# Optimization experiments

Hardware: AMD Instinct MI355X
Metric: run time of the kernel (lower is better)

Reference implementation:

```python
import jax, jax.numpy as jnp
import numpy as np

B, CIN, COUT, DK, DV, NH, H, W = 8, 256, 512, 256, 256, 8, 32, 32
DKH = DK // NH  # 32
DVH = DV // NH  # 32


def _conv(x, w, b, pad):
    y = jax.lax.conv_general_dilated(
        x, w, window_strides=(1, 1), padding=[(pad, pad), (pad, pad)],
        dimension_numbers=('NCHW', 'OIHW', 'NCHW'))
    return y + b[None, :, None, None]


def setup_inputs() -> dict:
    key = jax.random.key(0)
    ks = jax.random.split(key, 6)
    s = jnp.float32(0.05)
    return {
        'x': jax.random.normal(ks[0], (B, CIN, H, W), jnp.float32),
        'w_conv': jax.random.normal(ks[1], (COUT - DV, CIN, 3, 3), jnp.float32) * s,
        'b_conv': jnp.zeros((COUT - DV,), jnp.float32),
        'w_qkv': jax.random.normal(ks[2], (2 * DK + DV, CIN, 3, 3), jnp.float32) * s,
        'b_qkv': jnp.zeros((2 * DK + DV,), jnp.float32),
        'w_att': jax.random.normal(ks[3], (DV, DV, 1, 1), jnp.float32) * s,
        'b_att': jnp.zeros((DV,), jnp.float32),
        'key_rel_w': jax.random.normal(ks[4], (2 * W - 1, DKH), jnp.float32),
        'key_rel_h': jax.random.normal(ks[5], (2 * H - 1, DKH), jnp.float32),
    }


def reference(x, w_conv, b_conv, w_qkv, b_qkv, w_att, b_att, key_rel_w, key_rel_h):
    qkv = _conv(x, w_qkv, b_qkv, 1)                 # (B, 2*DK+DV, H, W)
    b = x.shape[0]
    q, k, v = qkv[:, :DK], qkv[:, DK:2 * DK], qkv[:, 2 * DK:]
    q = q.reshape(b, NH, DKH, H, W) * (DKH ** -0.5)
    kf = k.reshape(b, NH, DKH, H * W)
    vf = v.reshape(b, NH, DVH, H * W)
    qf = q.reshape(b, NH, DKH, H * W)
    # content logits: (B, NH, HW, HW)
    logits = jnp.einsum('bhdm,bhdn->bhmn', qf, kf)
    # relative position logits (equivalent to the pad/reshape/slice skew trick)
    q5 = jnp.transpose(q, (0, 1, 3, 4, 2))          # (B, NH, H, W, DKH)
    rel_w = jnp.einsum('bhxyd,md->bhxym', q5, key_rel_w)   # (B,NH,H,W,2W-1)
    idx_w = (jnp.arange(W)[None, :] - jnp.arange(W)[:, None]) + (W - 1)  # idx[y,y']
    rel_w = jnp.take_along_axis(rel_w, idx_w[None, None, None], axis=-1)  # (B,NH,H,W,W) [x,y,y']
    rel_h = jnp.einsum('bhxyd,md->bhxym', q5, key_rel_h)   # (B,NH,H,W,2H-1)
    idx_h = (jnp.arange(H)[None, :] - jnp.arange(H)[:, None]) + (H - 1)  # idx[x,x']
    rel_h = jnp.take_along_axis(rel_h, idx_h[None, None, :, None, :], axis=-1)  # (B,NH,H,W,H) [x,y,x']
    # logits6 axes: [x, y, x', y']
    logits6 = (logits.reshape(b, NH, H, W, H, W)
               + rel_w[:, :, :, :, None, :]
               + rel_h[:, :, :, :, :, None])
    weights = jax.nn.softmax(logits6.reshape(b, NH, H * W, H * W), axis=-1)
    att = jnp.einsum('bhmn,bhdn->bhmd', weights, vf)  # (B, NH, HW, DVH)
    # faithful to torch's contiguous .view(batch, dim_v, H, W)
    att = att.reshape(b, DV, H, W)
    att = _conv(att, w_att, b_att, 0)
    xo = _conv(x, w_conv, b_conv, 1)
    return jnp.concatenate([xo, att], axis=1)
```

## Files before the change

### kernel.cpp

```cpp
#include <hip/hip_runtime.h>


typedef __attribute__((ext_vector_type(8))) short short8;
typedef __attribute__((ext_vector_type(4))) float floatx4;

__device__ __forceinline__ unsigned short f2bf(float f) {
    unsigned int u = __float_as_uint(f);
    u += 0x7FFFu + ((u >> 16) & 1u);
    return (unsigned short)(u >> 16);
}
__device__ __forceinline__ float bf2f(unsigned short s) {
    return __uint_as_float(((unsigned int)s) << 16);
}
__device__ __forceinline__ unsigned int pk2bf_trunc(float lo, float hi) {
    return (__float_as_uint(lo) >> 16) | (__float_as_uint(hi) & 0xFFFF0000u);
}
__device__ __forceinline__ unsigned int pk2bf_rne(float lo, float hi) {
    return (unsigned int)f2bf(lo) | ((unsigned int)f2bf(hi) << 16);
}
__device__ __forceinline__ void gload_lds16(const unsigned short* g, unsigned short* s) {
    __builtin_amdgcn_global_load_lds(
        (const __attribute__((address_space(1))) unsigned int*)g,
        (__attribute__((address_space(3))) unsigned int*)s, 16, 0, 0);
}

__global__ __launch_bounds__(256) void k_xt(const float* __restrict__ x,
                                            unsigned short* __restrict__ Xt) {
    __shared__ unsigned short lds[256 * 33];
    const int tid = threadIdx.x;
    const int yy = blockIdx.x % 34;
    const int b  = blockIdx.x / 34;
    unsigned int* outp = (unsigned int*)(Xt + (((size_t)b * 34 + yy) * 34) * 256);
    if (yy == 0 || yy == 33) {
        for (int i = tid; i < 4352; i += 256) outp[i] = 0;
        return;
    }
    const int y = yy - 1;
    const float* xb = x + (size_t)b * 262144 + y * 32;
#pragma unroll
    for (int it = 0; it < 32; ++it) {
        const int e = it * 256 + tid;
        const int ci = e >> 5, xx = e & 31;
        lds[ci * 33 + xx] = f2bf(xb[ci * 1024 + xx]);
    }
    __syncthreads();
    const int ci2 = (tid & 127) * 2;
    const int xh = tid >> 7;
#pragma unroll
    for (int it = 0; it < 17; ++it) {
        const int xx = xh * 17 + it;
        unsigned int v = 0;
        if (xx >= 1 && xx <= 32)
            v = (unsigned int)lds[ci2 * 33 + xx - 1] |
                ((unsigned int)lds[(ci2 + 1) * 33 + xx - 1] << 16);
        outp[xx * 128 + (tid & 127)] = v;
    }
}

__global__ __launch_bounds__(256) void k_wconv(const float* __restrict__ wc,
                                               const float* __restrict__ wq,
                                               const float* __restrict__ wa,
                                               const float* __restrict__ krw,
                                               const float* __restrict__ krh,
                                               unsigned short* __restrict__ wt,
                                               unsigned short* __restrict__ wt2,
                                               unsigned short* __restrict__ krwb,
                                               unsigned short* __restrict__ krhb) {
    const int tid = threadIdx.x;
    const int blk = blockIdx.x;
    if (blk < 1024) {
        __shared__ float lw[2304];
        const int n = blk;
        const float* src = (n < 256) ? (wc + (size_t)n * 2304)
                                     : (wq + (size_t)(n - 256) * 2304);
#pragma unroll
        for (int it = 0; it < 9; ++it)
            lw[it * 256 + tid] = src[it * 256 + tid];
        __syncthreads();
#pragma unroll
        for (int it = 0; it < 9; ++it) {
            const int kp = it * 256 + tid;
            const int g = kp >> 8, ci = kp & 255;
            wt[(size_t)n * 2304 + kp] = f2bf(lw[ci * 9 + g]);
        }
    } else {
        const int i = (blk - 1024) * 256 + tid;
        if (i < 65536)        wt2[i] = f2bf(wa[i]);
        else if (i < 67584) { const int j = i - 65536;
                              krwb[j] = (j < 2016) ? f2bf(krw[j]) : (unsigned short)0; }
        else if (i < 69632) { const int j = i - 67584;
                              krhb[j] = (j < 2016) ? f2bf(krh[j]) : (unsigned short)0; }
    }
}

__global__ __launch_bounds__(256, 4) void k_gemm0(const unsigned short* __restrict__ Wr,
                                                  const unsigned short* __restrict__ Xt,
                                                  float* __restrict__ out,
                                                  unsigned short* __restrict__ qT,
                                                  unsigned short* __restrict__ kT,
                                                  unsigned short* __restrict__ vT,
                                                  const float* __restrict__ bias_a,
                                                  const float* __restrict__ bias_b) {
    __shared__ unsigned short As[64 * 64];
    __shared__ unsigned short Bs[128 * 64];
    const int tid = threadIdx.x;
    const int lane = tid & 63, wv = tid >> 6;
    const int l15 = lane & 15, quad = lane >> 4;
    const int m0 = blockIdx.x * 128, n0 = blockIdx.y * 64;
    const int wave_m = (wv & 1) * 64, wave_n = (wv >> 1) * 32;
    floatx4 acc[2][4] = {};
    const int lr = lane >> 3;
    const int swz8 = ((lane & 7) ^ lr) * 8;
    const unsigned short* gA = Wr + (size_t)(n0 + wv * 16 + lr) * 2304 + swz8;
    int bb0[4];
#pragma unroll
    for (int r = 0; r < 4; ++r) {
        const int m = m0 + wv * 32 + r * 8 + lr;
        const int b = m >> 10, p = m & 1023, y = p >> 5, x = p & 31;
        bb0[r] = ((b * 34 + y) * 34 + x) * 256;
    }
    unsigned short* sA0 = As + wv * 1024;
    unsigned short* sB0 = Bs + wv * 2048;
    const int sw0 = ((quad)     ^ (l15 & 7)) * 8;
    const int sw1 = ((4 + quad) ^ (l15 & 7)) * 8;
    for (int k0 = 0; k0 < 2304; k0 += 64) {
        const int g = k0 >> 8;
        const int ci0 = k0 & 255;
        const int ky = g / 3, kx = g - ky * 3;
        const int offu = (ky * 34 + kx) * 256 + ci0 + swz8;
        __syncthreads();
        gload_lds16(gA + k0, sA0);
        gload_lds16(gA + (size_t)8 * 2304 + k0, sA0 + 512);
#pragma unroll
        for (int r = 0; r < 4; ++r)
            gload_lds16(Xt + bb0[r] + offu, sB0 + r * 512);
        __syncthreads();
#pragma unroll
        for (int h = 0; h < 2; ++h) {
            const int sw = h ? sw1 : sw0;
            short8 a[2], b[4];
#pragma unroll
            for (int i = 0; i < 2; ++i)
                a[i] = *reinterpret_cast<const short8*>(As + (wave_n + i * 16 + l15) * 64 + sw);
#pragma unroll
            for (int j = 0; j < 4; ++j)
                b[j] = *reinterpret_cast<const short8*>(Bs + (wave_m + j * 16 + l15) * 64 + sw);
#pragma unroll
            for (int i = 0; i < 2; ++i)
#pragma unroll
                for (int j = 0; j < 4; ++j)
                    acc[i][j] = __builtin_amdgcn_mfma_f32_16x16x32_bf16(a[i], b[j], acc[i][j], 0, 0, 0);
        }
    }
#pragma unroll
    for (int i = 0; i < 2; ++i)
#pragma unroll
        for (int jj = 0; jj < 4; ++jj)
#pragma unroll
            for (int rg = 0; rg < 4; ++rg) {
                const int n = n0 + wave_n + i * 16 + quad * 4 + rg;
                const int m = m0 + wave_m + jj * 16 + l15;
                const float v = acc[i][jj][rg];
                const int bb = m >> 10, p = m & 1023;
                if (n < 256) {
                    out[(size_t)bb * 524288 + (size_t)n * 1024 + p] = v + bias_a[n];
                } else {
                    const int c = n - 256;
                    const float vq = v + bias_b[c];
                    if (c < 256) {
                        const int h = c >> 5, d = c & 31;
                        qT[(((size_t)(bb * 8 + h)) * 1024 + p) * 32 + d] =
                            f2bf(vq * 0.17677669529663687f);
                    } else if (c < 512) {
                        const int c2 = c - 256;
                        const int h = c2 >> 5, d = c2 & 31;
                        kT[(((size_t)(bb * 8 + h)) * 1024 + p) * 32 + d] = f2bf(vq);
                    } else {
                        const int c2 = c - 512;
                        const int h = c2 >> 5, d = c2 & 31;
                        vT[(((size_t)(bb * 8 + h)) * 32 + d) * 1024 + p] = f2bf(vq);
                    }
                }
            }
}

__global__ __launch_bounds__(256, 4) void k_attn(const unsigned short* __restrict__ qT,
                                                 const unsigned short* __restrict__ kT,
                                                 const unsigned short* __restrict__ vT,
                                                 const unsigned short* __restrict__ krwb,
                                                 const unsigned short* __restrict__ krhb,
                                                 unsigned short* __restrict__ attT) {
    __shared__ float rh_s[64 * 68];
    __shared__ unsigned short Pw[4 * 1152];
    const int tid = threadIdx.x;
    const int lane = tid & 63, wv = tid >> 6;
    const int l15 = lane & 15, quad = lane >> 4;
    const int bid = blockIdx.x;
    const int bh = bid & 63;
    const int qt = bid >> 6;
    const int h = bh & 7;
    const int b = bh >> 3;
    const unsigned short* qbase = qT + (size_t)bh * 32768;
    const unsigned short* kbase = kT + (size_t)bh * 32768;
    const unsigned short* vbase = vT + (size_t)bh * 32768;
    const int qloc = wv * 16 + l15;
    const int pq = qt * 64 + qloc;
    const int yq = pq >> 5, xq = pq & 31;

    const short8 qfrag = *reinterpret_cast<const short8*>(
        qbase + (size_t)pq * 32 + quad * 8);
    const floatx4 zero = {0.f, 0.f, 0.f, 0.f};
    unsigned short* pw = Pw + wv * 1152;

#pragma unroll
    for (int sub = 0; sub < 4; ++sub) {
        const short8 aw = *reinterpret_cast<const short8*>(krwb + (sub * 16 + l15) * 32 + quad * 8);
        const short8 ah = *reinterpret_cast<const short8*>(krhb + (sub * 16 + l15) * 32 + quad * 8);
        const floatx4 dw = __builtin_amdgcn_mfma_f32_16x16x32_bf16(aw, qfrag, zero, 0, 0, 0);
        const floatx4 dh = __builtin_amdgcn_mfma_f32_16x16x32_bf16(ah, qfrag, zero, 0, 0, 0);
        *reinterpret_cast<floatx4*>(rh_s + qloc * 68 + sub * 16 + quad * 4) = dh;
        uint2 uu;
        uu.x = pk2bf_rne(dw[0], dw[1]);
        uu.y = pk2bf_rne(dw[2], dw[3]);
        *reinterpret_cast<uint2*>(pw + l15 * 64 + sub * 16 + quad * 4) = uu;
    }
    float rwreg[8];
#pragma unroll
    for (int j = 0; j < 8; ++j) {
        const int xn = (j >> 2) * 16 + quad * 4 + (j & 3);
        rwreg[j] = bf2f(pw[l15 * 64 + xn - xq + 31]);
    }
    asm volatile("s_waitcnt lgkmcnt(0)" ::: "memory");

    const float* rhq = rh_s + qloc * 68 + 31 - yq;
    float lsum = 0.f;
    floatx4 O0 = zero, O1 = zero;

    short8 kf[4], vf[4];
#pragma unroll
    for (int sub = 0; sub < 4; ++sub)
        kf[sub] = *reinterpret_cast<const short8*>(
            kbase + (size_t)(sub * 16 + l15) * 32 + quad * 8);
#pragma unroll
    for (int n2 = 0; n2 < 2; ++n2) {
        vf[n2 * 2 + 0] = *reinterpret_cast<const short8*>(
            vbase + (size_t)l15 * 1024 + n2 * 32 + quad * 8);
        vf[n2 * 2 + 1] = *reinterpret_cast<const short8*>(
            vbase + (size_t)(16 + l15) * 1024 + n2 * 32 + quad * 8);
    }

#pragma unroll
    for (int nt = 0; nt < 16; ++nt) {
        const int n0 = nt * 64;
        const int n0n = (nt < 15) ? n0 + 64 : n0;
        floatx4 d[4];
#pragma unroll
        for (int sub = 0; sub < 4; ++sub)
            d[sub] = __builtin_amdgcn_mfma_f32_16x16x32_bf16(kf[sub], qfrag, zero, 0, 0, 0);
        short8 kfn[4], vfn[4];
#pragma unroll
        for (int sub = 0; sub < 4; ++sub)
            kfn[sub] = *reinterpret_cast<const short8*>(
                kbase + (size_t)(n0n + sub * 16 + l15) * 32 + quad * 8);
        const float rh0 = rhq[nt * 2];
        const float rh1 = rhq[nt * 2 + 1];
        float p[16];
#pragma unroll
        for (int sub = 0; sub < 4; ++sub) {
            const float rhv = (sub >> 1) ? rh1 : rh0;
#pragma unroll
            for (int r = 0; r < 4; ++r) {
                const float e = __expf(d[sub][r] + rwreg[(sub & 1) * 4 + r] + rhv);
                p[sub * 4 + r] = e;
                lsum += e;
            }
        }
#pragma unroll
        for (int sub = 0; sub < 4; ++sub) {
            uint2 uu;
            uu.x = pk2bf_trunc(p[sub * 4 + 0], p[sub * 4 + 1]);
            uu.y = pk2bf_trunc(p[sub * 4 + 2], p[sub * 4 + 3]);
            *reinterpret_cast<uint2*>(pw + l15 * 72 + sub * 16 + quad * 4) = uu;
        }
        asm volatile("s_waitcnt lgkmcnt(0)" ::: "memory");
#pragma unroll
        for (int n2 = 0; n2 < 2; ++n2) {
            const short8 pfrag = *reinterpret_cast<const short8*>(
                pw + l15 * 72 + n2 * 32 + quad * 8);
            O0 = __builtin_amdgcn_mfma_f32_16x16x32_bf16(vf[n2 * 2 + 0], pfrag, O0, 0, 0, 0);
            O1 = __builtin_amdgcn_mfma_f32_16x16x32_bf16(vf[n2 * 2 + 1], pfrag, O1, 0, 0, 0);
        }
#pragma unroll
        for (int n2 = 0; n2 < 2; ++n2) {
            vfn[n2 * 2 + 0] = *reinterpret_cast<const short8*>(
                vbase + (size_t)l15 * 1024 + n0n + n2 * 32 + quad * 8);
            vfn[n2 * 2 + 1] = *reinterpret_cast<const short8*>(
                vbase + (size_t)(16 + l15) * 1024 + n0n + n2 * 32 + quad * 8);
        }
#pragma unroll
        for (int i = 0; i < 4; ++i) { kf[i] = kfn[i]; vf[i] = vfn[i]; }
    }
    lsum += __shfl_xor(lsum, 16);
    lsum += __shfl_xor(lsum, 32);
    const float inv = 1.0f / lsum;
    unsigned short* ob = attT + ((size_t)(h * 32 + yq)) * 8192 + b * 1024 + xq * 32;
    uint2 o0, o1;
    o0.x = pk2bf_rne(O0[0] * inv, O0[1] * inv);
    o0.y = pk2bf_rne(O0[2] * inv, O0[3] * inv);
    o1.x = pk2bf_rne(O1[0] * inv, O1[1] * inv);
    o1.y = pk2bf_rne(O1[2] * inv, O1[3] * inv);
    *reinterpret_cast<uint2*>(ob + quad * 4) = o0;
    *reinterpret_cast<uint2*>(ob + 16 + quad * 4) = o1;
}

__global__ __launch_bounds__(256) void k_tr(const unsigned short* __restrict__ src,
                                            unsigned short* __restrict__ dst) {
    __shared__ unsigned short t[64 * 72];
    const int tid = threadIdx.x;
    const int m0 = (blockIdx.x & 127) * 64;
    const int k0 = (blockIdx.x >> 7) * 64;
#pragma unroll
    for (int i = 0; i < 2; ++i) {
        const int idx = i * 256 + tid;
        const int k = idx >> 3, c8 = (idx & 7) * 8;
        *reinterpret_cast<uint4*>(t + k * 72 + c8) =
            *reinterpret_cast<const uint4*>(src + (size_t)(k0 + k) * 8192 + m0 + c8);
    }
    __syncthreads();
#pragma unroll
    for (int i = 0; i < 2; ++i) {
        const int idx = i * 256 + tid;
        const int m = idx >> 3, c8 = (idx & 7) * 8;
        unsigned short v[8];
#pragma unroll
        for (int j = 0; j < 8; ++j) v[j] = t[(c8 + j) * 72 + m];
        *reinterpret_cast<uint4*>(dst + (size_t)(m0 + m) * 256 + k0 + c8) =
            *reinterpret_cast<uint4*>(v);
    }
}

__global__ __launch_bounds__(256) void k_gemm_s(const unsigned short* __restrict__ Wm,
                                                const unsigned short* __restrict__ Dm,
                                                float* __restrict__ out,
                                                const float* __restrict__ bias) {
    __shared__ unsigned short As[64 * 40];
    __shared__ unsigned short Bs[64 * 40];
    const int tid = threadIdx.x;
    const int m0 = blockIdx.x * 64, n0 = blockIdx.y * 64;
    const int lane = tid & 63;
    const int wv = tid >> 6;
    const int l15 = lane & 15, quad = lane >> 4;
    const int n_off = (wv & 1) * 32, m_off = (wv >> 1) * 32;
    floatx4 acc[2][2] = {};
    const int r = tid >> 2, c8 = (tid & 3) * 8;
    const unsigned short* gA = Wm + (size_t)(n0 + r) * 256 + c8;
    const unsigned short* gB = Dm + (size_t)(m0 + r) * 256 + c8;
    unsigned short* sA = As + r * 40 + c8;
    unsigned short* sB = Bs + r * 40 + c8;
    for (int k0 = 0; k0 < 256; k0 += 32) {
        __syncthreads();
        *reinterpret_cast<uint4*>(sA) = *reinterpret_cast<const uint4*>(gA + k0);
        *reinterpret_cast<uint4*>(sB) = *reinterpret_cast<const uint4*>(gB + k0);
        __syncthreads();
        const short8 a0 = *reinterpret_cast<const short8*>(As + (n_off +      l15) * 40 + quad * 8);
        const short8 a1 = *reinterpret_cast<const short8*>(As + (n_off + 16 + l15) * 40 + quad * 8);
        const short8 b0 = *reinterpret_cast<const short8*>(Bs + (m_off +      l15) * 40 + quad * 8);
        const short8 b1 = *reinterpret_cast<const short8*>(Bs + (m_off + 16 + l15) * 40 + quad * 8);
        acc[0][0] = __builtin_amdgcn_mfma_f32_16x16x32_bf16(a0, b0, acc[0][0], 0, 0, 0);
        acc[0][1] = __builtin_amdgcn_mfma_f32_16x16x32_bf16(a0, b1, acc[0][1], 0, 0, 0);
        acc[1][0] = __builtin_amdgcn_mfma_f32_16x16x32_bf16(a1, b0, acc[1][0], 0, 0, 0);
        acc[1][1] = __builtin_amdgcn_mfma_f32_16x16x32_bf16(a1, b1, acc[1][1], 0, 0, 0);
    }
#pragma unroll
    for (int i = 0; i < 2; ++i)
#pragma unroll
        for (int jj = 0; jj < 2; ++jj)
#pragma unroll
            for (int rg = 0; rg < 4; ++rg) {
                const int n = n0 + n_off + i * 16 + quad * 4 + rg;
                const int m = m0 + m_off + jj * 16 + l15;
                const int bb = m >> 10, p = m & 1023;
                out[(size_t)bb * 524288 + (size_t)(n + 256) * 1024 + p] =
                    acc[i][jj][rg] + bias[n];
            }
}

extern "C" void kernel_launch(void* const* d_in, const int* in_sizes, int n_in,
                              void* d_out, int out_size, void* d_ws, size_t ws_size,
                              hipStream_t stream) {
    const float* x      = (const float*)d_in[0];
    const float* w_conv = (const float*)d_in[1];
    const float* b_conv = (const float*)d_in[2];
    const float* w_qkv  = (const float*)d_in[3];
    const float* b_qkv  = (const float*)d_in[4];
    const float* w_att  = (const float*)d_in[5];
    const float* b_att  = (const float*)d_in[6];
    const float* krw    = (const float*)d_in[7];
    const float* krh    = (const float*)d_in[8];
    float* out = (float*)d_out;

    char* ws = (char*)d_ws;
    unsigned short* Xt    = (unsigned short*)(ws);
    unsigned short* wt    = (unsigned short*)(ws + 9470464);
    unsigned short* wt2   = (unsigned short*)(ws + 14189056);
    unsigned short* qT    = (unsigned short*)(ws + 14320128);
    unsigned short* kT    = (unsigned short*)(ws + 18514432);
    unsigned short* vT    = (unsigned short*)(ws + 22708736);
    unsigned short* attt  = (unsigned short*)(ws + 26903040);
    unsigned short* krwb  = (unsigned short*)(ws + 31097344);
    unsigned short* krhb  = (unsigned short*)(ws + 31101440);
    unsigned short* attTT = (unsigned short*)(ws + 31105536);

    k_xt<<<dim3(272), dim3(256), 0, stream>>>(x, Xt);
    k_wconv<<<dim3(1296), dim3(256), 0, stream>>>(w_conv, w_qkv, w_att, krw, krh,
                                                  wt, wt2, krwb, krhb);
    k_gemm0<<<dim3(64, 16), dim3(256), 0, stream>>>(wt, Xt, out, qT, kT, vT,
                                                    b_conv, b_qkv);
    k_attn<<<dim3(1024), dim3(256), 0, stream>>>(qT, kT, vT, krwb, krhb, attTT);
    k_tr<<<dim3(512), dim3(256), 0, stream>>>(attTT, attt);
    k_gemm_s<<<dim3(128, 4), dim3(256), 0, stream>>>(wt2, attt, out, b_att);
}
```

Measured before the change: 196.5 us.

## Merge prep kernels and process two key tiles per attention iteration

```diff
diff --git a/kernel.cpp b/kernel.cpp
--- a/kernel.cpp
+++ b/kernel.cpp
@@ -24,53 +24,52 @@
         (__attribute__((address_space(3))) unsigned int*)s, 16, 0, 0);
 }
 
-__global__ __launch_bounds__(256) void k_xt(const float* __restrict__ x,
-                                            unsigned short* __restrict__ Xt) {
-    __shared__ unsigned short lds[256 * 33];
-    const int tid = threadIdx.x;
-    const int yy = blockIdx.x % 34;
-    const int b  = blockIdx.x / 34;
-    unsigned int* outp = (unsigned int*)(Xt + (((size_t)b * 34 + yy) * 34) * 256);
-    if (yy == 0 || yy == 33) {
-        for (int i = tid; i < 4352; i += 256) outp[i] = 0;
-        return;
-    }
-    const int y = yy - 1;
-    const float* xb = x + (size_t)b * 262144 + y * 32;
-#pragma unroll
-    for (int it = 0; it < 32; ++it) {
-        const int e = it * 256 + tid;
-        const int ci = e >> 5, xx = e & 31;
-        lds[ci * 33 + xx] = f2bf(xb[ci * 1024 + xx]);
-    }
-    __syncthreads();
-    const int ci2 = (tid & 127) * 2;
-    const int xh = tid >> 7;
-#pragma unroll
-    for (int it = 0; it < 17; ++it) {
-        const int xx = xh * 17 + it;
-        unsigned int v = 0;
-        if (xx >= 1 && xx <= 32)
-            v = (unsigned int)lds[ci2 * 33 + xx - 1] |
-                ((unsigned int)lds[(ci2 + 1) * 33 + xx - 1] << 16);
-        outp[xx * 128 + (tid & 127)] = v;
-    }
-}
-
-__global__ __launch_bounds__(256) void k_wconv(const float* __restrict__ wc,
-                                               const float* __restrict__ wq,
-                                               const float* __restrict__ wa,
-                                               const float* __restrict__ krw,
-                                               const float* __restrict__ krh,
-                                               unsigned short* __restrict__ wt,
-                                               unsigned short* __restrict__ wt2,
-                                               unsigned short* __restrict__ krwb,
-                                               unsigned short* __restrict__ krhb) {
+__global__ __launch_bounds__(256) void k_prep(const float* __restrict__ x,
+                                              const float* __restrict__ wc,
+                                              const float* __restrict__ wq,
+                                              const float* __restrict__ wa,
+                                              const float* __restrict__ krw,
+                                              const float* __restrict__ krh,
+                                              unsigned short* __restrict__ Xt,
+                                              unsigned short* __restrict__ wt,
+                                              unsigned short* __restrict__ wt2,
+                                              unsigned short* __restrict__ krwb,
+                                              unsigned short* __restrict__ krhb) {
+    __shared__ char smem[16896];
     const int tid = threadIdx.x;
     const int blk = blockIdx.x;
-    if (blk < 1024) {
-        __shared__ float lw[2304];
-        const int n = blk;
+    if (blk < 272) {
+        unsigned short* lds = (unsigned short*)smem;
+        const int yy = blk % 34;
+        const int b  = blk / 34;
+        unsigned int* outp = (unsigned int*)(Xt + (((size_t)b * 34 + yy) * 34) * 256);
+        if (yy == 0 || yy == 33) {
+            for (int i = tid; i < 4352; i += 256) outp[i] = 0;
+            return;
+        }
+        const int y = yy - 1;
+        const float* xb = x + (size_t)b * 262144 + y * 32;
+#pragma unroll
+        for (int it = 0; it < 32; ++it) {
+            const int e = it * 256 + tid;
+            const int ci = e >> 5, xx = e & 31;
+            lds[ci * 33 + xx] = f2bf(xb[ci * 1024 + xx]);
+        }
+        __syncthreads();
+        const int ci2 = (tid & 127) * 2;
+        const int xh = tid >> 7;
+#pragma unroll
+        for (int it = 0; it < 17; ++it) {
+            const int xx = xh * 17 + it;
+            unsigned int v = 0;
+            if (xx >= 1 && xx <= 32)
+                v = (unsigned int)lds[ci2 * 33 + xx - 1] |
+                    ((unsigned int)lds[(ci2 + 1) * 33 + xx - 1] << 16);
+            outp[xx * 128 + (tid & 127)] = v;
+        }
+    } else if (blk < 1296) {
+        float* lw = (float*)smem;
+        const int n = blk - 272;
         const float* src = (n < 256) ? (wc + (size_t)n * 2304)
                                      : (wq + (size_t)(n - 256) * 2304);
 #pragma unroll
@@ -84,7 +83,7 @@
             wt[(size_t)n * 2304 + kp] = f2bf(lw[ci * 9 + g]);
         }
     } else {
-        const int i = (blk - 1024) * 256 + tid;
+        const int i = (blk - 1296) * 256 + tid;
         if (i < 65536)        wt2[i] = f2bf(wa[i]);
         else if (i < 67584) { const int j = i - 65536;
                               krwb[j] = (j < 2016) ? f2bf(krw[j]) : (unsigned short)0; }
@@ -191,7 +190,7 @@
                                                  const unsigned short* __restrict__ krhb,
                                                  unsigned short* __restrict__ attT) {
     __shared__ float rh_s[64 * 68];
-    __shared__ unsigned short Pw[4 * 1152];
+    __shared__ unsigned short Pw[4 * 2304];
     const int tid = threadIdx.x;
     const int lane = tid & 63, wv = tid >> 6;
     const int l15 = lane & 15, quad = lane >> 4;
@@ -210,7 +209,8 @@
     const short8 qfrag = *reinterpret_cast<const short8*>(
         qbase + (size_t)pq * 32 + quad * 8);
     const floatx4 zero = {0.f, 0.f, 0.f, 0.f};
-    unsigned short* pw = Pw + wv * 1152;
+    unsigned short* pwA = Pw + wv * 2304;
+    unsigned short* pwB = pwA + 1152;
 
 #pragma unroll
     for (int sub = 0; sub < 4; ++sub) {
@@ -222,13 +222,13 @@
         uint2 uu;
         uu.x = pk2bf_rne(dw[0], dw[1]);
         uu.y = pk2bf_rne(dw[2], dw[3]);
-        *reinterpret_cast<uint2*>(pw + l15 * 64 + sub * 16 + quad * 4) = uu;
+        *reinterpret_cast<uint2*>(pwA + l15 * 64 + sub * 16 + quad * 4) = uu;
     }
     float rwreg[8];
 #pragma unroll
     for (int j = 0; j < 8; ++j) {
         const int xn = (j >> 2) * 16 + quad * 4 + (j & 3);
-        rwreg[j] = bf2f(pw[l15 * 64 + xn - xq + 31]);
+        rwreg[j] = bf2f(pwA[l15 * 64 + xn - xq + 31]);
     }
     asm volatile("s_waitcnt lgkmcnt(0)" ::: "memory");
 
@@ -236,69 +236,89 @@
     float lsum = 0.f;
     floatx4 O0 = zero, O1 = zero;
 
-    short8 kf[4], vf[4];
-#pragma unroll
-    for (int sub = 0; sub < 4; ++sub)
-        kf[sub] = *reinterpret_cast<const short8*>(
+    short8 kfa[4], kfb[4], vfa[4], vfb[4];
+#pragma unroll
+    for (int sub = 0; sub < 4; ++sub) {
+        kfa[sub] = *reinterpret_cast<const short8*>(
             kbase + (size_t)(sub * 16 + l15) * 32 + quad * 8);
-#pragma unroll
-    for (int n2 = 0; n2 < 2; ++n2) {
-        vf[n2 * 2 + 0] = *reinterpret_cast<const short8*>(
-            vbase + (size_t)l15 * 1024 + n2 * 32 + quad * 8);
-        vf[n2 * 2 + 1] = *reinterpret_cast<const short8*>(
-            vbase + (size_t)(16 + l15) * 1024 + n2 * 32 + quad * 8);
-    }
-
-#pragma unroll
-    for (int nt = 0; nt < 16; ++nt) {
-        const int n0 = nt * 64;
-        const int n0n = (nt < 15) ? n0 + 64 : n0;
-        floatx4 d[4];
+        kfb[sub] = *reinterpret_cast<const short8*>(
+            kbase + (size_t)(64 + sub * 16 + l15) * 32 + quad * 8);
+    }
+    vfa[0] = *reinterpret_cast<const short8*>(vbase + (size_t)l15 * 1024 + quad * 8);
+    vfa[1] = *reinterpret_cast<const short8*>(vbase + (size_t)(16 + l15) * 1024 + quad * 8);
+    vfa[2] = *reinterpret_cast<const short8*>(vbase + (size_t)l15 * 1024 + 32 + quad * 8);
+    vfa[3] = *reinterpret_cast<const short8*>(vbase + (size_t)(16 + l15) * 1024 + 32 + quad * 8);
+    vfb[0] = *reinterpret_cast<const short8*>(vbase + (size_t)l15 * 1024 + 64 + quad * 8);
+    vfb[1] = *reinterpret_cast<const short8*>(vbase + (size_t)(16 + l15) * 1024 + 64 + quad * 8);
+    vfb[2] = *reinterpret_cast<const short8*>(vbase + (size_t)l15 * 1024 + 96 + quad * 8);
+    vfb[3] = *reinterpret_cast<const short8*>(vbase + (size_t)(16 + l15) * 1024 + 96 + quad * 8);
+
+    for (int it = 0; it < 8; ++it) {
+        const int n0a = it * 128;
+        floatx4 da[4], db[4];
 #pragma unroll
         for (int sub = 0; sub < 4; ++sub)
-            d[sub] = __builtin_amdgcn_mfma_f32_16x16x32_bf16(kf[sub], qfrag, zero, 0, 0, 0);
-        short8 kfn[4], vfn[4];
+            da[sub] = __builtin_amdgcn_mfma_f32_16x16x32_bf16(kfa[sub], qfrag, zero, 0, 0, 0);
 #pragma unroll
         for (int sub = 0; sub < 4; ++sub)
-            kfn[sub] = *reinterpret_cast<const short8*>(
-                kbase + (size_t)(n0n + sub * 16 + l15) * 32 + quad * 8);
-        const float rh0 = rhq[nt * 2];
-        const float rh1 = rhq[nt * 2 + 1];
-        float p[16];
+            db[sub] = __builtin_amdgcn_mfma_f32_16x16x32_bf16(kfb[sub], qfrag, zero, 0, 0, 0);
+        const int nk = (it < 7) ? n0a + 128 : n0a;
 #pragma unroll
         for (int sub = 0; sub < 4; ++sub) {
-            const float rhv = (sub >> 1) ? rh1 : rh0;
-#pragma unroll
-            for (int r = 0; r < 4; ++r) {
-                const float e = __expf(d[sub][r] + rwreg[(sub & 1) * 4 + r] + rhv);
-                p[sub * 4 + r] = e;
-                lsum += e;
-            }
-        }
+            kfa[sub] = *reinterpret_cast<const short8*>(
+                kbase + (size_t)(nk + sub * 16 + l15) * 32 + quad * 8);
+            kfb[sub] = *reinterpret_cast<const short8*>(
+                kbase + (size_t)(nk + 64 + sub * 16 + l15) * 32 + quad * 8);
+        }
+        const float rhA0 = rhq[it * 4],     rhA1 = rhq[it * 4 + 1];
+        const float rhB0 = rhq[it * 4 + 2], rhB1 = rhq[it * 4 + 3];
 #pragma unroll
         for (int sub = 0; sub < 4; ++sub) {
+            const float rhv = (sub >> 1) ? rhA1 : rhA0;
+            const float p0 = __expf(da[sub][0] + rwreg[(sub & 1) * 4 + 0] + rhv);
+            const float p1 = __expf(da[sub][1] + rwreg[(sub & 1) * 4 + 1] + rhv);
+            const float p2 = __expf(da[sub][2] + rwreg[(sub & 1) * 4 + 2] + rhv);
+            const float p3 = __expf(da[sub][3] + rwreg[(sub & 1) * 4 + 3] + rhv);
+            lsum += (p0 + p1) + (p2 + p3);
             uint2 uu;
-            uu.x = pk2bf_trunc(p[sub * 4 + 0], p[sub * 4 + 1]);
-            uu.y = pk2bf_trunc(p[sub * 4 + 2], p[sub * 4 + 3]);
-            *reinterpret_cast<uint2*>(pw + l15 * 72 + sub * 16 + quad * 4) = uu;
+            uu.x = pk2bf_trunc(p0, p1);
+            uu.y = pk2bf_trunc(p2, p3);
+            *reinterpret_cast<uint2*>(pwA + l15 * 72 + sub * 16 + quad * 4) = uu;
+        }
+#pragma unroll
+        for (int sub = 0; sub < 4; ++sub) {
+            const float rhv = (sub >> 1) ? rhB1 : rhB0;
+            const float p0 = __expf(db[sub][0] + rwreg[(sub & 1) * 4 + 0] + rhv);
+            const float p1 = __expf(db[sub][1] + rwreg[(sub & 1) * 4 + 1] + rhv);
+            const float p2 = __expf(db[sub][2] + rwreg[(sub & 1) * 4 + 2] + rhv);
+            const float p3 = __expf(db[sub][3] + rwreg[(sub & 1) * 4 + 3] + rhv);
+            lsum += (p0 + p1) + (p2 + p3);
+            uint2 uu;
+            uu.x = pk2bf_trunc(p0, p1);
+            uu.y = pk2bf_trunc(p2, p3);
+            *reinterpret_cast<uint2*>(pwB + l15 * 72 + sub * 16 + quad * 4) = uu;
         }
         asm volatile("s_waitcnt lgkmcnt(0)" ::: "memory");
-#pragma unroll
-        for (int n2 = 0; n2 < 2; ++n2) {
-            const short8 pfrag = *reinterpret_cast<const short8*>(
-                pw + l15 * 72 + n2 * 32 + quad * 8);
-            O0 = __builtin_amdgcn_mfma_f32_16x16x32_bf16(vf[n2 * 2 + 0], pfrag, O0, 0, 0, 0);
-            O1 = __builtin_amdgcn_mfma_f32_16x16x32_bf16(vf[n2 * 2 + 1], pfrag, O1, 0, 0, 0);
-        }
-#pragma unroll
-        for (int n2 = 0; n2 < 2; ++n2) {
-            vfn[n2 * 2 + 0] = *reinterpret_cast<const short8*>(
-                vbase + (size_t)l15 * 1024 + n0n + n2 * 32 + quad * 8);
-            vfn[n2 * 2 + 1] = *reinterpret_cast<const short8*>(
-                vbase + (size_t)(16 + l15) * 1024 + n0n + n2 * 32 + quad * 8);
-        }
-#pragma unroll
-        for (int i = 0; i < 4; ++i) { kf[i] = kfn[i]; vf[i] = vfn[i]; }
+        const short8 pfa0 = *reinterpret_cast<const short8*>(pwA + l15 * 72 + quad * 8);
+        const short8 pfa1 = *reinterpret_cast<const short8*>(pwA + l15 * 72 + 32 + quad * 8);
+        const short8 pfb0 = *reinterpret_cast<const short8*>(pwB + l15 * 72 + quad * 8);
+        const short8 pfb1 = *reinterpret_cast<const short8*>(pwB + l15 * 72 + 32 + quad * 8);
+        O0 = __builtin_amdgcn_mfma_f32_16x16x32_bf16(vfa[0], pfa0, O0, 0, 0, 0);
+        O1 = __builtin_amdgcn_mfma_f32_16x16x32_bf16(vfa[1], pfa0, O1, 0, 0, 0);
+        O0 = __builtin_amdgcn_mfma_f32_16x16x32_bf16(vfa[2], pfa1, O0, 0, 0, 0);
+        O1 = __builtin_amdgcn_mfma_f32_16x16x32_bf16(vfa[3], pfa1, O1, 0, 0, 0);
+        O0 = __builtin_amdgcn_mfma_f32_16x16x32_bf16(vfb[0], pfb0, O0, 0, 0, 0);
+        O1 = __builtin_amdgcn_mfma_f32_16x16x32_bf16(vfb[1], pfb0, O1, 0, 0, 0);
+        O0 = __builtin_amdgcn_mfma_f32_16x16x32_bf16(vfb[2], pfb1, O0, 0, 0, 0);
+        O1 = __builtin_amdgcn_mfma_f32_16x16x32_bf16(vfb[3], pfb1, O1, 0, 0, 0);
+        vfa[0] = *reinterpret_cast<const short8*>(vbase + (size_t)l15 * 1024 + nk + quad * 8);
+        vfa[1] = *reinterpret_cast<const short8*>(vbase + (size_t)(16 + l15) * 1024 + nk + quad * 8);
+        vfa[2] = *reinterpret_cast<const short8*>(vbase + (size_t)l15 * 1024 + nk + 32 + quad * 8);
+        vfa[3] = *reinterpret_cast<const short8*>(vbase + (size_t)(16 + l15) * 1024 + nk + 32 + quad * 8);
+        vfb[0] = *reinterpret_cast<const short8*>(vbase + (size_t)l15 * 1024 + nk + 64 + quad * 8);
+        vfb[1] = *reinterpret_cast<const short8*>(vbase + (size_t)(16 + l15) * 1024 + nk + 64 + quad * 8);
+        vfb[2] = *reinterpret_cast<const short8*>(vbase + (size_t)l15 * 1024 + nk + 96 + quad * 8);
+        vfb[3] = *reinterpret_cast<const short8*>(vbase + (size_t)(16 + l15) * 1024 + nk + 96 + quad * 8);
     }
     lsum += __shfl_xor(lsum, 16);
     lsum += __shfl_xor(lsum, 32);
@@ -411,9 +431,8 @@
     unsigned short* krhb  = (unsigned short*)(ws + 31101440);
     unsigned short* attTT = (unsigned short*)(ws + 31105536);
 
-    k_xt<<<dim3(272), dim3(256), 0, stream>>>(x, Xt);
-    k_wconv<<<dim3(1296), dim3(256), 0, stream>>>(w_conv, w_qkv, w_att, krw, krh,
-                                                  wt, wt2, krwb, krhb);
+    k_prep<<<dim3(1568), dim3(256), 0, stream>>>(x, w_conv, w_qkv, w_att, krw, krh,
+                                                 Xt, wt, wt2, krwb, krhb);
     k_gemm0<<<dim3(64, 16), dim3(256), 0, stream>>>(wt, Xt, out, qT, kT, vT,
                                                     b_conv, b_qkv);
     k_attn<<<dim3(1024), dim3(256), 0, stream>>>(qT, kT, vT, krwb, krhb, attTT);
```

Result: slower. 202.8 us (+3.2%).

## Stage attention K/V through double-buffered LDS and merge prep kernels

Applied to the files above, without the earlier changes.

```diff
diff --git a/kernel.cpp b/kernel.cpp
--- a/kernel.cpp
+++ b/kernel.cpp
@@ -24,53 +24,52 @@
         (__attribute__((address_space(3))) unsigned int*)s, 16, 0, 0);
 }
 
-__global__ __launch_bounds__(256) void k_xt(const float* __restrict__ x,
-                                            unsigned short* __restrict__ Xt) {
-    __shared__ unsigned short lds[256 * 33];
-    const int tid = threadIdx.x;
-    const int yy = blockIdx.x % 34;
-    const int b  = blockIdx.x / 34;
-    unsigned int* outp = (unsigned int*)(Xt + (((size_t)b * 34 + yy) * 34) * 256);
-    if (yy == 0 || yy == 33) {
-        for (int i = tid; i < 4352; i += 256) outp[i] = 0;
-        return;
-    }
-    const int y = yy - 1;
-    const float* xb = x + (size_t)b * 262144 + y * 32;
-#pragma unroll
-    for (int it = 0; it < 32; ++it) {
-        const int e = it * 256 + tid;
-        const int ci = e >> 5, xx = e & 31;
-        lds[ci * 33 + xx] = f2bf(xb[ci * 1024 + xx]);
-    }
-    __syncthreads();
-    const int ci2 = (tid & 127) * 2;
-    const int xh = tid >> 7;
-#pragma unroll
-    for (int it = 0; it < 17; ++it) {
-        const int xx = xh * 17 + it;
-        unsigned int v = 0;
-        if (xx >= 1 && xx <= 32)
-            v = (unsigned int)lds[ci2 * 33 + xx - 1] |
-                ((unsigned int)lds[(ci2 + 1) * 33 + xx - 1] << 16);
-        outp[xx * 128 + (tid & 127)] = v;
-    }
-}
-
-__global__ __launch_bounds__(256) void k_wconv(const float* __restrict__ wc,
-                                               const float* __restrict__ wq,
-                                               const float* __restrict__ wa,
-                                               const float* __restrict__ krw,
-                                               const float* __restrict__ krh,
-                                               unsigned short* __restrict__ wt,
-                                               unsigned short* __restrict__ wt2,
-                                               unsigned short* __restrict__ krwb,
-                                               unsigned short* __restrict__ krhb) {
+__global__ __launch_bounds__(256) void k_prep(const float* __restrict__ x,
+                                              const float* __restrict__ wc,
+                                              const float* __restrict__ wq,
+                                              const float* __restrict__ wa,
+                                              const float* __restrict__ krw,
+                                              const float* __restrict__ krh,
+                                              unsigned short* __restrict__ Xt,
+                                              unsigned short* __restrict__ wt,
+                                              unsigned short* __restrict__ wt2,
+                                              unsigned short* __restrict__ krwb,
+                                              unsigned short* __restrict__ krhb) {
+    __shared__ char smem[16896];
     const int tid = threadIdx.x;
     const int blk = blockIdx.x;
-    if (blk < 1024) {
-        __shared__ float lw[2304];
-        const int n = blk;
+    if (blk < 272) {
+        unsigned short* lds = (unsigned short*)smem;
+        const int yy = blk % 34;
+        const int b  = blk / 34;
+        unsigned int* outp = (unsigned int*)(Xt + (((size_t)b * 34 + yy) * 34) * 256);
+        if (yy == 0 || yy == 33) {
+            for (int i = tid; i < 4352; i += 256) outp[i] = 0;
+            return;
+        }
+        const int y = yy - 1;
+        const float* xb = x + (size_t)b * 262144 + y * 32;
+#pragma unroll
+        for (int it = 0; it < 32; ++it) {
+            const int e = it * 256 + tid;
+            const int ci = e >> 5, xx = e & 31;
+            lds[ci * 33 + xx] = f2bf(xb[ci * 1024 + xx]);
+        }
+        __syncthreads();
+        const int ci2 = (tid & 127) * 2;
+        const int xh = tid >> 7;
+#pragma unroll
+        for (int it = 0; it < 17; ++it) {
+            const int xx = xh * 17 + it;
+            unsigned int v = 0;
+            if (xx >= 1 && xx <= 32)
+                v = (unsigned int)lds[ci2 * 33 + xx - 1] |
+                    ((unsigned int)lds[(ci2 + 1) * 33 + xx - 1] << 16);
+            outp[xx * 128 + (tid & 127)] = v;
+        }
+    } else if (blk < 1296) {
+        float* lw = (float*)smem;
+        const int n = blk - 272;
         const float* src = (n < 256) ? (wc + (size_t)n * 2304)
                                      : (wq + (size_t)(n - 256) * 2304);
 #pragma unroll
@@ -84,7 +83,7 @@
             wt[(size_t)n * 2304 + kp] = f2bf(lw[ci * 9 + g]);
         }
     } else {
-        const int i = (blk - 1024) * 256 + tid;
+        const int i = (blk - 1296) * 256 + tid;
         if (i < 65536)        wt2[i] = f2bf(wa[i]);
         else if (i < 67584) { const int j = i - 65536;
                               krwb[j] = (j < 2016) ? f2bf(krw[j]) : (unsigned short)0; }
@@ -184,12 +183,14 @@
             }
 }
 
-__global__ __launch_bounds__(256, 4) void k_attn(const unsigned short* __restrict__ qT,
+__global__ __launch_bounds__(256, 3) void k_attn(const unsigned short* __restrict__ qT,
                                                  const unsigned short* __restrict__ kT,
                                                  const unsigned short* __restrict__ vT,
                                                  const unsigned short* __restrict__ krwb,
                                                  const unsigned short* __restrict__ krhb,
                                                  unsigned short* __restrict__ attT) {
+    __shared__ unsigned short Ks[2][2048];
+    __shared__ unsigned short Vs[2][2048];
     __shared__ float rh_s[64 * 68];
     __shared__ unsigned short Pw[4 * 1152];
     const int tid = threadIdx.x;
@@ -212,6 +213,15 @@
     const floatx4 zero = {0.f, 0.f, 0.f, 0.f};
     unsigned short* pw = Pw + wv * 1152;
 
+    const int lr8 = lane >> 3, lc8 = lane & 7;
+    const int swz = (lc8 ^ lr8) * 8;
+    const unsigned short* ksrc = kbase + wv * 512 + lr8 * 64 + swz;
+    const unsigned short* vsrc = vbase + (size_t)(wv * 8 + lr8) * 1024 + swz;
+    unsigned short* kdst0 = &Ks[0][wv * 512];
+    unsigned short* kdst1 = &Ks[1][wv * 512];
+    unsigned short* vdst0 = &Vs[0][wv * 512];
+    unsigned short* vdst1 = &Vs[1][wv * 512];
+
 #pragma unroll
     for (int sub = 0; sub < 4; ++sub) {
         const short8 aw = *reinterpret_cast<const short8*>(krwb + (sub * 16 + l15) * 32 + quad * 8);
@@ -236,81 +246,80 @@
     float lsum = 0.f;
     floatx4 O0 = zero, O1 = zero;
 
-    short8 kf[4], vf[4];
-#pragma unroll
-    for (int sub = 0; sub < 4; ++sub)
-        kf[sub] = *reinterpret_cast<const short8*>(
-            kbase + (size_t)(sub * 16 + l15) * 32 + quad * 8);
-#pragma unroll
-    for (int n2 = 0; n2 < 2; ++n2) {
-        vf[n2 * 2 + 0] = *reinterpret_cast<const short8*>(
-            vbase + (size_t)l15 * 1024 + n2 * 32 + quad * 8);
-        vf[n2 * 2 + 1] = *reinterpret_cast<const short8*>(
-            vbase + (size_t)(16 + l15) * 1024 + n2 * 32 + quad * 8);
-    }
-
-#pragma unroll
+    gload_lds16(ksrc, kdst0);
+    gload_lds16(vsrc, vdst0);
+    __syncthreads();
+
+    const int krow = (l15 >> 1);
+    const int kchunkbase = (l15 & 1) * 4;
+    const int vsw0 = ((quad)     ^ (l15 & 7)) * 8;
+    const int vsw1 = ((4 + quad) ^ (l15 & 7)) * 8;
+
     for (int nt = 0; nt < 16; ++nt) {
-        const int n0 = nt * 64;
-        const int n0n = (nt < 15) ? n0 + 64 : n0;
+        const unsigned short* Kc = Ks[nt & 1];
+        const unsigned short* Vc = Vs[nt & 1];
+        if (nt < 15) {
+            gload_lds16(ksrc + (nt + 1) * 2048, (nt & 1) ? kdst0 : kdst1);
+            gload_lds16(vsrc + (nt + 1) * 64,  (nt & 1) ? vdst0 : vdst1);
+        }
         floatx4 d[4];
 #pragma unroll
-        for (int sub = 0; sub < 4; ++sub)
-            d[sub] = __builtin_amdgcn_mfma_f32_16x16x32_bf16(kf[sub], qfrag, zero, 0, 0, 0);
-        short8 kfn[4], vfn[4];
-#pragma unroll
-        for (int sub = 0; sub < 4; ++sub)
-            kfn[sub] = *reinterpret_cast<const short8*>(
-                kbase + (size_t)(n0n + sub * 16 + l15) * 32 + quad * 8);
+        for (int sub = 0; sub < 4; ++sub) {
+            const int row = sub * 8 + krow;
+            const short8 kf = *reinterpret_cast<const short8*>(
+                Kc + row * 64 + ((kchunkbase + quad) ^ krow) * 8);
+            d[sub] = __builtin_amdgcn_mfma_f32_16x16x32_bf16(kf, qfrag, zero, 0, 0, 0);
+        }
         const float rh0 = rhq[nt * 2];
         const float rh1 = rhq[nt * 2 + 1];
-        float p[16];
 #pragma unroll
         for (int sub = 0; sub < 4; ++sub) {
             const float rhv = (sub >> 1) ? rh1 : rh0;
-#pragma unroll
-            for (int r = 0; r < 4; ++r) {
-                const float e = __expf(d[sub][r] + rwreg[(sub & 1) * 4 + r] + rhv);
-                p[sub * 4 + r] = e;
-                lsum += e;
-            }
-        }
-#pragma unroll
-        for (int sub = 0; sub < 4; ++sub) {
+            const float p0 = __expf(d[sub][0] + rwreg[(sub & 1) * 4 + 0] + rhv);
+            const float p1 = __expf(d[sub][1] + rwreg[(sub & 1) * 4 + 1] + rhv);
+            const float p2 = __expf(d[sub][2] + rwreg[(sub & 1) * 4 + 2] + rhv);
+            const float p3 = __expf(d[sub][3] + rwreg[(sub & 1) * 4 + 3] + rhv);
+            lsum += (p0 + p1) + (p2 + p3);
             uint2 uu;
-            uu.x = pk2bf_trunc(p[sub * 4 + 0], p[sub * 4 + 1]);
-            uu.y = pk2bf_trunc(p[sub * 4 + 2], p[sub * 4 + 3]);
+            uu.x = pk2bf_trunc(p0, p1);
+            uu.y = pk2bf_trunc(p2, p3);
             *reinterpret_cast<uint2*>(pw + l15 * 72 + sub * 16 + quad * 4) = uu;
         }
         asm volatile("s_waitcnt lgkmcnt(0)" ::: "memory");
-#pragma unroll
-        for (int n2 = 0; n2 < 2; ++n2) {
-            const short8 pfrag = *reinterpret_cast<const short8*>(
-                pw + l15 * 72 + n2 * 32 + quad * 8);
-            O0 = __builtin_amdgcn_mfma_f32_16x16x32_bf16(vf[n2 * 2 + 0], pfrag, O0, 0, 0, 0);
-            O1 = __builtin_amdgcn_mfma_f32_16x16x32_bf16(vf[n2 * 2 + 1], pfrag, O1, 0, 0, 0);
-        }
-#pragma unroll
-        for (int n2 = 0; n2 < 2; ++n2) {
-            vfn[n2 * 2 + 0] = *reinterpret_cast<const short8*>(
-                vbase + (size_t)l15 * 1024 + n0n + n2 * 32 + quad * 8);
-            vfn[n2 * 2 + 1] = *reinterpret_cast<const short8*>(
-                vbase + (size_t)(16 + l15) * 1024 + n0n + n2 * 32 + quad * 8);
-        }
-#pragma unroll
-        for (int i = 0; i < 4; ++i) { kf[i] = kfn[i]; vf[i] = vfn[i]; }
+        const short8 pf0 = *reinterpret_cast<const short8*>(pw + l15 * 72 + quad * 8);
+        const short8 pf1 = *reinterpret_cast<const short8*>(pw + l15 * 72 + 32 + quad * 8);
+        const short8 vf0 = *reinterpret_cast<const short8*>(Vc + l15 * 64 + vsw0);
+        const short8 vf1 = *reinterpret_cast<const short8*>(Vc + (16 + l15) * 64 + vsw0);
+        const short8 vf2 = *reinterpret_cast<const short8*>(Vc + l15 * 64 + vsw1);
+        const short8 vf3 = *reinterpret_cast<const short8*>(Vc + (16 + l15) * 64 + vsw1);
+        O0 = __builtin_amdgcn_mfma_f32_16x16x32_bf16(vf0, pf0, O0, 0, 0, 0);
+        O1 = __builtin_amdgcn_mfma_f32_16x16x32_bf16(vf1, pf0, O1, 0, 0, 0);
+        O0 = __builtin_amdgcn_mfma_f32_16x16x32_bf16(vf2, pf1, O0, 0, 0, 0);
+        O1 = __builtin_amdgcn_mfma_f32_16x16x32_bf16(vf3, pf1, O1, 0, 0, 0);
+        __syncthreads();
     }
     lsum += __shfl_xor(lsum, 16);
     lsum += __shfl_xor(lsum, 32);
     const float inv = 1.0f / lsum;
-    unsigned short* ob = attT + ((size_t)(h * 32 + yq)) * 8192 + b * 1024 + xq * 32;
-    uint2 o0, o1;
-    o0.x = pk2bf_rne(O0[0] * inv, O0[1] * inv);
-    o0.y = pk2bf_rne(O0[2] * inv, O0[3] * inv);
-    o1.x = pk2bf_rne(O1[0] * inv, O1[1] * inv);
-    o1.y = pk2bf_rne(O1[2] * inv, O1[3] * inv);
-    *reinterpret_cast<uint2*>(ob + quad * 4) = o0;
-    *reinterpret_cast<uint2*>(ob + 16 + quad * 4) = o1;
+    unsigned short* Ob = &Ks[0][0];
+    {
+        const int row = wv >> 1;
+        const int xql = (wv & 1) * 16 + l15;
+        uint2 o0, o1;
+        o0.x = pk2bf_rne(O0[0] * inv, O0[1] * inv);
+        o0.y = pk2bf_rne(O0[2] * inv, O0[3] * inv);
+        o1.x = pk2bf_rne(O1[0] * inv, O1[1] * inv);
+        o1.y = pk2bf_rne(O1[2] * inv, O1[3] * inv);
+        *reinterpret_cast<uint2*>(Ob + row * 1024 + xql * 32 + quad * 4) = o0;
+        *reinterpret_cast<uint2*>(Ob + row * 1024 + xql * 32 + 16 + quad * 4) = o1;
+    }
+    __syncthreads();
+    {
+        const int row = tid >> 7, c16 = tid & 127;
+        *reinterpret_cast<uint4*>(
+            attT + ((size_t)(h * 32 + qt * 2 + row)) * 8192 + b * 1024 + c16 * 8) =
+            *reinterpret_cast<const uint4*>(Ob + row * 1024 + c16 * 8);
+    }
 }
 
 __global__ __launch_bounds__(256) void k_tr(const unsigned short* __restrict__ src,
@@ -411,9 +420,8 @@
     unsigned short* krhb  = (unsigned short*)(ws + 31101440);
     unsigned short* attTT = (unsigned short*)(ws + 31105536);
 
-    k_xt<<<dim3(272), dim3(256), 0, stream>>>(x, Xt);
-    k_wconv<<<dim3(1296), dim3(256), 0, stream>>>(w_conv, w_qkv, w_att, krw, krh,
-                                                  wt, wt2, krwb, krhb);
+    k_prep<<<dim3(1568), dim3(256), 0, stream>>>(x, w_conv, w_qkv, w_att, krw, krh,
+                                                 Xt, wt, wt2, krwb, krhb);
     k_gemm0<<<dim3(64, 16), dim3(256), 0, stream>>>(wt, Xt, out, qT, kT, vT,
                                                     b_conv, b_qkv);
     k_attn<<<dim3(1024), dim3(256), 0, stream>>>(qT, kT, vT, krwb, krhb, attTT);
```

Measured after the change: 178.4 us. 1.1x faster.
